# Kernel optimization log

Measured on AMD Instinct MI355X. Metric: run time of the kernel, lower is better.

Reference implementation:

```python
import jax, jax.numpy as jnp
import numpy as np
from functools import lru_cache
from jax.scipy.linalg import expm

N_QUBITS = 6
DIM = 2 ** N_QUBITS          # 64
N_PAULI = 4 ** N_QUBITS      # 4096


@lru_cache(maxsize=None)
def _pauli_tensor_np(n_qubits):
    # All n-qubit Pauli strings as dense matrices, ordered base-4
    # (digit 0..3 -> I, X, Y, Z; most-significant digit = first qubit).
    I = np.eye(2, dtype=np.complex64)
    X = np.array([[0, 1], [1, 0]], dtype=np.complex64)
    Y = np.array([[0, -1j], [1j, 0]], dtype=np.complex64)
    Z = np.array([[1, 0], [0, -1]], dtype=np.complex64)
    base = np.stack([I, X, Y, Z])  # [4,2,2]
    T = base
    for _ in range(n_qubits - 1):
        k, d = T.shape[0], T.shape[1]
        T = np.einsum('iab,jcd->ijacbd', T, base).reshape(k * 4, d * 2, d * 2)
    return np.ascontiguousarray(T.astype(np.complex64))  # [4^n, 2^n, 2^n]


def setup_inputs() -> dict:
    key = jax.random.key(0)
    kx, kw, kb = jax.random.split(key, 3)
    x = jax.random.normal(kx, (512, 4000), dtype=jnp.float32)
    weight = jax.random.normal(kw, (4, N_PAULI - 1), dtype=jnp.float32)
    bias = jax.random.normal(kb, (DIM,), dtype=jnp.float32)
    return {"x": x, "weight": weight, "bias": bias}


def reference(x, weight, bias):
    # x: [B, in_dim] float32; weight: [n_reps, 4^n - 1]; bias: [out_dim]
    B, in_dim = x.shape
    n_reps = weight.shape[0]
    out_dim = bias.shape[0]
    P = jnp.asarray(_pauli_tensor_np(N_QUBITS))  # [4096, 64, 64] complex64

    # Pad data coefficients up to the full Pauli basis (identity included).
    xp = jnp.pad(x, ((0, 0), (0, N_PAULI - in_dim))).astype(jnp.complex64)

    # Data-encoding Hamiltonian per sample: H_d[b] = sum_p x[b,p] * P[p]
    Hd = jnp.einsum('bp,pij->bij', xp, P)                       # [B,64,64]
    Ud = jax.vmap(expm)(-1j * Hd)                               # [B,64,64]

    # Trainable Hamiltonians per rep (identity Pauli excluded -> global phase).
    Hp = jnp.einsum('rp,pij->rij', weight.astype(jnp.complex64), P[1:])
    Up = jax.vmap(expm)(-1j * Hp)                               # [R,64,64]

    # Data re-uploading circuit on |0...0>: repeat (U_param @ U_data).
    psi = jnp.zeros((B, DIM), dtype=jnp.complex64).at[:, 0].set(1.0)
    for r in range(n_reps):
        psi = jnp.einsum('bij,bj->bi', Ud, psi)
        psi = jnp.einsum('ij,bj->bi', Up[r], psi)

    # Observables are computational-basis projectors |k><k|, k < out_dim:
    # <psi|O_k|psi> = |psi_k|^2
    probs = (psi[:, :out_dim].real ** 2 + psi[:, :out_dim].imag ** 2)
    return probs.astype(jnp.float32) + bias
```

## Files before the change

### kernel.cpp

```cpp
#include <hip/hip_runtime.h>
#include <math.h>

typedef float2 cplx;
typedef __attribute__((ext_vector_type(8))) short short8v;
typedef __attribute__((ext_vector_type(4))) short short4v;
typedef __attribute__((ext_vector_type(4))) float float4v;

#define IN_DIM 4000
#define NREPS 4

#define C0f  1.0f
#define C1f  1.0f
#define C2f  0.5f
#define C3f  0.16666667f
#define C4f  0.041666668f
#define C5f  8.3333333e-3f
#define C6f  1.3888889e-3f
#define C7f  1.9841270e-4f
#define C8f  2.4801587e-5f
#define C9f  2.7557319e-6f
#define C10f 2.7557319e-7f
#define C11f 2.5052108e-8f
#define C12f 2.0876757e-9f
#define C13f 1.6059044e-10f
#define C14f 1.1470746e-11f
#define C15f 7.6471637e-13f

#define MFMA(A,B,C) __builtin_amdgcn_mfma_f32_16x16x32_bf16((A),(B),(C),0,0,0)


__device__ __forceinline__ int idxSw(int a, int b) {
    return (a << 6) + ((((b >> 3) + a) & 7) << 3) + (b & 7);
}
__device__ __forceinline__ short f2bf(float f) {
    unsigned u = __float_as_uint(f);
    return (short)((u + 0x7FFF + ((u >> 16) & 1)) >> 16);
}
__device__ __forceinline__ float bf2f(short s) {
    return __uint_as_float(((unsigned)(unsigned short)s) << 16);
}
__device__ __forceinline__ short8v neg8(short8v a) {
    int4 u; __builtin_memcpy(&u, &a, 16);
    u.x ^= 0x80008000; u.y ^= 0x80008000; u.z ^= 0x80008000; u.w ^= 0x80008000;
    short8v r; __builtin_memcpy(&r, &u, 16); return r;
}

template<int AM, int BM, int ND>
__device__ __forceinline__ void mm_mfma(const short* __restrict__ As,
                                        const short* __restrict__ Bs,
                                        int li, int q, int mb, int nb,
                                        float4v* __restrict__ accR,
                                        float4v* __restrict__ accI)
{
    #pragma unroll
    for (int ks = 0; ks < 2; ks++) {
        const int ch = ks * 4 + q;
        short8v arh[ND], arl[ND], cRh[ND], cRl[ND], cIh[ND], cIl[ND];
        #pragma unroll
        for (int dm = 0; dm < ND; dm++) {
            int r = ((mb + dm) << 4) + li;
            int off = (r << 6) + (((ch + r) & 7) << 3);
            arh[dm] = *(const short8v*)(As + off);
            arl[dm] = *(const short8v*)(As + 4096 + off);
            short8v aih = *(const short8v*)(As + 8192 + off);
            short8v ail = *(const short8v*)(As + 12288 + off);
            short8v nih = neg8(aih), nil_ = neg8(ail);
            cRh[dm] = (AM == 2) ? aih : nih;
            cRl[dm] = (AM == 2) ? ail : nil_;
            cIh[dm] = (AM == 2) ? nih : aih;
            cIl[dm] = (AM == 2) ? nil_ : ail;
        }
        #pragma unroll
        for (int dn = 0; dn < ND; dn++) {
            int n = ((nb + dn) << 4) + li;
            int off = (n << 6) + (((ch + n) & 7) << 3);
            short8v brh = *(const short8v*)(Bs + off);
            short8v brl = *(const short8v*)(Bs + 4096 + off);
            short8v bih = *(const short8v*)(Bs + 8192 + off);
            short8v bil = *(const short8v*)(Bs + 12288 + off);
            if (BM == 1) { brh = neg8(brh); brl = neg8(brl); }
            #pragma unroll
            for (int dm = 0; dm < ND; dm++) {
                int ti = dm * ND + dn;
                accR[ti] = MFMA(arh[dm], brh, accR[ti]);
                accR[ti] = MFMA(arh[dm], brl, accR[ti]);
                accR[ti] = MFMA(arl[dm], brh, accR[ti]);
                accR[ti] = MFMA(cRh[dm], bih, accR[ti]);
                accR[ti] = MFMA(cRh[dm], bil, accR[ti]);
                accR[ti] = MFMA(cRl[dm], bih, accR[ti]);
                accI[ti] = MFMA(arh[dm], bih, accI[ti]);
                accI[ti] = MFMA(arh[dm], bil, accI[ti]);
                accI[ti] = MFMA(arl[dm], bih, accI[ti]);
                accI[ti] = MFMA(cIh[dm], brh, accI[ti]);
                accI[ti] = MFMA(cIh[dm], brl, accI[ti]);
                accI[ti] = MFMA(cIl[dm], brh, accI[ti]);
            }
        }
    }
}

template<int ND>
__device__ __forceinline__ void write_row(short* __restrict__ S, int li, int q,
                                          int mb, int nb,
                                          const float4v* cre, const float4v* cim)
{
    #pragma unroll
    for (int dm = 0; dm < ND; dm++)
    #pragma unroll
    for (int dn = 0; dn < ND; dn++) {
        int ti = dm * ND + dn;
        int c = ((nb + dn) << 4) + li;
        #pragma unroll
        for (int reg = 0; reg < 4; reg++) {
            int r = ((mb + dm) << 4) + q * 4 + reg;
            int off = idxSw(r, c);
            float vr = cre[ti][reg], vi = cim[ti][reg];
            short rh = f2bf(vr), rl = f2bf(vr - bf2f(rh));
            short ih = f2bf(vi), il = f2bf(vi - bf2f(ih));
            S[off] = rh; S[4096 + off] = rl; S[8192 + off] = ih; S[12288 + off] = il;
        }
    }
}

template<int ND>
__device__ __forceinline__ void write_rowT(short* __restrict__ S, int li, int q,
                                           int mb, int nb,
                                           const float4v* cre, const float4v* cim)
{
    #pragma unroll
    for (int dm = 0; dm < ND; dm++)
    #pragma unroll
    for (int dn = 0; dn < ND; dn++) {
        int ti = dm * ND + dn;
        int c = ((nb + dn) << 4) + li;
        int k0 = ((mb + dm) << 4) + q * 4;
        int off = idxSw(c, k0);
        short4v rh, rl, ih, il;
        #pragma unroll
        for (int reg = 0; reg < 4; reg++) {
            float vr = cre[ti][reg], vi = cim[ti][reg];
            short h1 = f2bf(vr); rh[reg] = h1; rl[reg] = f2bf(vr - bf2f(h1));
            short h2 = f2bf(vi); ih[reg] = h2; il[reg] = f2bf(vi - bf2f(h2));
        }
        *(short4v*)(S + off) = rh;
        *(short4v*)(S + 4096 + off) = rl;
        *(short4v*)(S + 8192 + off) = ih;
        *(short4v*)(S + 12288 + off) = il;
    }
}

template<int ND>
__device__ __forceinline__ void gather_tile(const short* __restrict__ S, int li, int q,
                                            int mb, int nb, float4v* bre, float4v* bim)
{
    #pragma unroll
    for (int dm = 0; dm < ND; dm++)
    #pragma unroll
    for (int dn = 0; dn < ND; dn++) {
        int ti = dm * ND + dn;
        int c = ((nb + dn) << 4) + li;
        #pragma unroll
        for (int reg = 0; reg < 4; reg++) {
            int r = ((mb + dm) << 4) + q * 4 + reg;
            int off = idxSw(r, c);
            bre[ti][reg] = bf2f(S[off]) + bf2f(S[4096 + off]);
            bim[ti][reg] = bf2f(S[8192 + off]) + bf2f(S[12288 + off]);
        }
    }
}

template<int ND>
__device__ __forceinline__ void adddiag(float4v* u, float cI, int li, int q, int mb, int nb)
{
    #pragma unroll
    for (int dm = 0; dm < ND; dm++)
    #pragma unroll
    for (int dn = 0; dn < ND; dn++) {
        if (mb + dm == nb + dn) {
            #pragma unroll
            for (int e = 0; e < 4; e++)
                if (li == q * 4 + e) u[dm * ND + dn][e] += cI;
        }
    }
}

template<int ND>
__device__ __forceinline__ void store_tiles(cplx* __restrict__ dst, int li, int q,
                                            int mb, int nb,
                                            const float4v* ure, const float4v* uim)
{
    #pragma unroll
    for (int dm = 0; dm < ND; dm++)
    #pragma unroll
    for (int dn = 0; dn < ND; dn++) {
        int ti = dm * ND + dn;
        int c = ((nb + dn) << 4) + li;
        int cs = c ^ (((c >> 4) & 1) << 1);
        #pragma unroll
        for (int reg = 0; reg < 4; reg++) {
            int r = ((mb + dm) << 4) + q * 4 + reg;
            dst[(r << 6) + cs] = make_float2(ure[ti][reg], uim[ti][reg]);
        }
    }
}

__device__ __forceinline__ cplx pauli_phase(float v, int xm, int zm) {
    int ny = __popc(xm & zm) & 3;
    if (ny == 0) return make_float2(v, 0.f);
    if (ny == 1) return make_float2(0.f, -v);
    if (ny == 2) return make_float2(-v, 0.f);
    return make_float2(0.f, v);
}

__device__ __forceinline__ void expm_core4(char* __restrict__ LDS,
                                           const float* __restrict__ src, bool isW,
                                           int t, float4v* ure, float4v* uim)
{
    constexpr int ND = 2, NT = 4;
    short* S0 = (short*)LDS;
    short* S1 = (short*)(LDS + 32768);
    cplx*  W  = (cplx*)(LDS + 32768);
    float* red = (float*)(LDS + 65536);
    const int lane = t & 63, wv = t >> 6;
    const int li = lane & 15, q = lane >> 4;
    const int mb = (wv & 1) << 1, nb = (wv >> 1) << 1;

    int xmt = 0, zmt = 0;
    #pragma unroll
    for (int k = 0; k < 6; k++) {
        int lo = (t >> (2 * k)) & 1, hi = (t >> (2 * k + 1)) & 1;
        zmt |= hi << k; xmt |= (hi ^ lo) << k;
    }
    float sumsq = 0.f;
    #pragma unroll
    for (int n = 0; n < 16; n++) {
        int p = t + 256 * n;
        int lo0 = n & 1, hi0 = (n >> 1) & 1, lo1 = (n >> 2) & 1, hi1 = (n >> 3) & 1;
        int zmn = hi0 | (hi1 << 1), xmn = (hi0 ^ lo0) | ((hi1 ^ lo1) << 1);
        int xm = xmt | (xmn << 4), zm = zmt | (zmn << 4);
        float v = isW ? ((p == 0) ? 0.f : src[p - 1])
                      : ((p < IN_DIM) ? src[p] : 0.f);
        sumsq += v * v;
        W[(xm << 6) + zm] = pauli_phase(v, xm, zm);
    }
    #pragma unroll
    for (int d = 32; d >= 1; d >>= 1) sumsq += __shfl_xor(sumsq, d, 64);
    if (lane == 0) red[wv] = sumsq;
    __syncthreads();

    float rs = 0.f;
    #pragma unroll
    for (int i2 = 0; i2 < 4; i2++) rs += red[i2];
    float fro = sqrtf(64.f * rs);
    int s1 = 0; { float nn = fro; while (nn > 8.f && s1 < 24) { nn *= 0.5f; s1++; } }
    float sc1 = exp2f((float)(-s1));

    cplx hv[16];
    #pragma unroll
    for (int rr = 0; rr < 16; rr++) hv[rr] = W[((wv * 16 + rr) << 6) + lane];
    #pragma unroll
    for (int d = 1; d < 64; d <<= 1) {
        float sg = (lane & d) ? -1.f : 1.f;
        #pragma unroll
        for (int rr = 0; rr < 16; rr++) {
            float px = __shfl_xor(hv[rr].x, d, 64);
            float py = __shfl_xor(hv[rr].y, d, 64);
            hv[rr].x = fmaf(sg, hv[rr].x, px);
            hv[rr].y = fmaf(sg, hv[rr].y, py);
        }
    }

    #pragma unroll
    for (int rr = 0; rr < 16; rr++) {
        int m = wv * 16 + rr;
        int c = lane ^ m;
        float vr = hv[rr].y * sc1, vi = -hv[rr].x * sc1;
        short rh = f2bf(vr), rl = f2bf(vr - bf2f(rh));
        short ih = f2bf(vi), il = f2bf(vi - bf2f(ih));
        int off = idxSw(lane, c);
        S0[off] = rh; S0[4096 + off] = rl; S0[8192 + off] = ih; S0[12288 + off] = il;
    }
    __syncthreads();

    const float4v z4 = {0.f, 0.f, 0.f, 0.f};
    float4v accR[NT], accI[NT];
    #define ZERO_ACC _Pragma("unroll") for (int i2 = 0; i2 < NT; i2++) { accR[i2]=z4; accI[i2]=z4; }

    ZERO_ACC
    mm_mfma<0, 1, ND>(S0, S0, li, q, mb, nb, accR, accI);
    float ss = 0.f;
    #pragma unroll
    for (int ti = 0; ti < NT; ti++)
        #pragma unroll
        for (int e = 0; e < 4; e++)
            ss += accR[ti][e]*accR[ti][e] + accI[ti][e]*accI[ti][e];
    #pragma unroll
    for (int d = 32; d >= 1; d >>= 1) ss += __shfl_xor(ss, d, 64);
    if (lane == 0) red[4 + wv] = ss;
    __syncthreads();

    rs = 0.f;
    #pragma unroll
    for (int i2 = 0; i2 < 4; i2++) rs += red[4 + i2];
    float bound = sqrtf(sqrtf(rs));
    int ds = 0; { float nn = bound; while (nn > 3.4f && ds < 12) { nn *= 0.5f; ds++; } }
    const int s = s1 + ds;
    float dsc = exp2f((float)(-ds)), dsc2 = dsc * dsc;

    float4v bre[NT], bim[NT];
    gather_tile<ND>(S0, li, q, mb, nb, bre, bim);
    float4v a2r[NT], a2i[NT];
    #pragma unroll
    for (int ti = 0; ti < NT; ti++) { a2r[ti] = accR[ti] * dsc2; a2i[ti] = accI[ti] * dsc2; }
    write_rowT<ND>(S1, li, q, mb, nb, a2r, a2i);
    __syncthreads();

    ZERO_ACC
    mm_mfma<2, 1, ND>(S1, S0, li, q, mb, nb, accR, accI);
    float4v a3r[NT], a3i[NT];
    #pragma unroll
    for (int ti = 0; ti < NT; ti++) { a3r[ti] = accR[ti] * dsc; a3i[ti] = accI[ti] * dsc; }
    ZERO_ACC
    mm_mfma<2, 0, ND>(S1, S1, li, q, mb, nb, accR, accI);
    __syncthreads();
    write_rowT<ND>(S0, li, q, mb, nb, accR, accI);
    {
        float caA = C13f * dsc, ca3 = C15f * dsc;
        #pragma unroll
        for (int ti = 0; ti < NT; ti++) {
            ure[ti] = caA * bre[ti] + C14f * a2r[ti] + ca3 * a3r[ti];
            uim[ti] = caA * bim[ti] + C14f * a2i[ti] + ca3 * a3i[ti];
        }
        adddiag<ND>(ure, C12f, li, q, mb, nb);
        write_row<ND>(S1, li, q, mb, nb, ure, uim);
    }
    __syncthreads();

    const float cIc[3] = { C0f, C4f, C8f };
    const float cAc[3] = { C1f, C5f, C9f };
    const float c2c[3] = { C2f, C6f, C10f };
    const float c3c[3] = { C3f, C7f, C11f };
    for (int j = 2; j >= 0; j--) {
        ZERO_ACC
        mm_mfma<0, 0, ND>(S1, S0, li, q, mb, nb, accR, accI);
        __syncthreads();
        float caA = cAc[j] * dsc, ca3 = c3c[j] * dsc;
        #pragma unroll
        for (int ti = 0; ti < NT; ti++) {
            ure[ti] = accR[ti] + caA * bre[ti] + c2c[j] * a2r[ti] + ca3 * a3r[ti];
            uim[ti] = accI[ti] + caA * bim[ti] + c2c[j] * a2i[ti] + ca3 * a3i[ti];
        }
        adddiag<ND>(ure, cIc[j], li, q, mb, nb);
        write_row<ND>(S1, li, q, mb, nb, ure, uim);
        if (j == 0) write_rowT<ND>(S0, li, q, mb, nb, ure, uim);
        __syncthreads();
    }

    for (int sq = 0; sq < s; sq++) {
        if (sq > 0) {
            write_row<ND>(S1, li, q, mb, nb, ure, uim);
            write_rowT<ND>(S0, li, q, mb, nb, ure, uim);
            __syncthreads();
        }
        ZERO_ACC
        mm_mfma<0, 0, ND>(S1, S0, li, q, mb, nb, accR, accI);
        __syncthreads();
        #pragma unroll
        for (int ti = 0; ti < NT; ti++) { ure[ti] = accR[ti]; uim[ti] = accI[ti]; }
    }
    #undef ZERO_ACC
}

__device__ __forceinline__ cplx matvec_wave(const cplx* __restrict__ M,
                                            const cplx* __restrict__ pin,
                                            int lane, int wv)
{
    const int rr = (wv << 4) + (lane & 15);
    const int kc = lane >> 4;
    float ax = 0.f, ay = 0.f;
    const float4* Mr = (const float4*)(M + (rr << 6));
    #pragma unroll
    for (int c = 0; c < 4; c++) {
        int ch = ((kc << 2) + c + rr) & 15;
        int b = (ch >> 2) & 1;
        float4 m01 = Mr[(ch << 1) + b];
        float4 m23 = Mr[(ch << 1) + 1 - b];
        const cplx* p = pin + (ch << 2);
        cplx p0 = p[0], p1 = p[1], p2 = p[2], p3 = p[3];
        ax = fmaf(m01.x, p0.x, fmaf(-m01.y, p0.y, ax));
        ay = fmaf(m01.x, p0.y, fmaf( m01.y, p0.x, ay));
        ax = fmaf(m01.z, p1.x, fmaf(-m01.w, p1.y, ax));
        ay = fmaf(m01.z, p1.y, fmaf( m01.w, p1.x, ay));
        ax = fmaf(m23.x, p2.x, fmaf(-m23.y, p2.y, ax));
        ay = fmaf(m23.x, p2.y, fmaf( m23.y, p2.x, ay));
        ax = fmaf(m23.z, p3.x, fmaf(-m23.w, p3.y, ax));
        ay = fmaf(m23.z, p3.y, fmaf( m23.w, p3.x, ay));
    }
    ax += __shfl_xor(ax, 16, 64); ay += __shfl_xor(ay, 16, 64);
    ax += __shfl_xor(ax, 32, 64); ay += __shfl_xor(ay, 32, 64);
    return make_float2(ax, ay);
}

__global__ __launch_bounds__(256, 2) void circuit_kernel(const float* __restrict__ x,
                                                         const float* __restrict__ w,
                                                         const float* __restrict__ bias,
                                                         cplx* __restrict__ ws,
                                                         int* __restrict__ flag,
                                                         float* __restrict__ out)
{
    __shared__ float4 LDSf4[4168];
    char* LDS = (char*)LDSf4;
    const int t = threadIdx.x, b = blockIdx.x;
    const int lane = t & 63, wv = t >> 6, li = lane & 15, q = lane >> 4;
    float4v ure[4], uim[4];

    if (b < NREPS) {
        expm_core4(LDS, w + (size_t)b * 4095, true, t, ure, uim);
        store_tiles<2>(ws + ((size_t)b << 12), li, q, (wv & 1) << 1, (wv >> 1) << 1,
                       ure, uim);
        __syncthreads();
        if (t == 0)
            __hip_atomic_fetch_add(flag, 1, __ATOMIC_RELEASE, __HIP_MEMORY_SCOPE_AGENT);
    }

    expm_core4(LDS, x + (size_t)b * IN_DIM, false, t, ure, uim);

    cplx* Ud   = (cplx*)(LDS + 32768);
    cplx* UpS  = (cplx*)LDS;
    cplx* psiA = (cplx*)(LDS + 65664);
    cplx* psiB = (cplx*)(LDS + 66176);

    store_tiles<2>(Ud, li, q, (wv & 1) << 1, (wv >> 1) << 1, ure, uim);
    if (t < 64) psiA[t] = make_float2(t == 0 ? 1.f : 0.f, 0.f);
    if (t == 0) {
        while (__hip_atomic_load(flag, __ATOMIC_ACQUIRE, __HIP_MEMORY_SCOPE_AGENT) < NREPS)
            __builtin_amdgcn_s_sleep(8);
    }
    __syncthreads();

    const int rowi = (wv << 4) + (lane & 15);
    for (int r = 0; r < NREPS; r++) {
        {
            const float4* srcv = (const float4*)(ws + ((size_t)r << 12));
            float4* dstY = (float4*)UpS;
            #pragma unroll
            for (int n = 0; n < 8; n++) dstY[n * 256 + t] = srcv[n * 256 + t];
        }
        cplx v1 = matvec_wave(Ud, psiA, lane, wv);
        if (lane < 16) psiB[rowi] = v1;
        __syncthreads();
        cplx v2 = matvec_wave(UpS, psiB, lane, wv);
        if (lane < 16) psiA[rowi] = v2;
        __syncthreads();
    }
    if (t < 64) {
        cplx pv = psiA[t];
        out[(b << 6) + t] = fmaf(pv.x, pv.x, fmaf(pv.y, pv.y, bias[t]));
    }
}

extern "C" void kernel_launch(void* const* d_in, const int* in_sizes, int n_in,
                              void* d_out, int out_size, void* d_ws, size_t ws_size,
                              hipStream_t stream)
{
    const float* x    = (const float*)d_in[0];
    const float* w    = (const float*)d_in[1];
    const float* bias = (const float*)d_in[2];
    float* out = (float*)d_out;
    cplx* ws   = (cplx*)d_ws;
    int* flag  = (int*)((char*)d_ws + (NREPS << 15));

    int B = in_sizes[0] / IN_DIM;

    hipMemsetAsync(flag, 0, sizeof(int), stream);
    hipLaunchKernelGGL(circuit_kernel, dim3(B), dim3(256), 0, stream,
                       x, w, bias, ws, flag, out);
}
```

Measured before the change: 166.6 us.

## Use Horner Taylor evaluation in expm, add MFMA priority, loop expm duties

Measured after the change: 197.7 us. +18.7%, slower.

```diff
diff --git a/kernel.cpp b/kernel.cpp
--- a/kernel.cpp
+++ b/kernel.cpp
@@ -79,6 +79,7 @@
             short8v bih = *(const short8v*)(Bs + 8192 + off);
             short8v bil = *(const short8v*)(Bs + 12288 + off);
             if (BM == 1) { brh = neg8(brh); brl = neg8(brl); }
+            __builtin_amdgcn_s_setprio(1);
             #pragma unroll
             for (int dm = 0; dm < ND; dm++) {
                 int ti = dm * ND + dn;
@@ -95,6 +96,7 @@
                 accI[ti] = MFMA(cIh[dm], brl, accI[ti]);
                 accI[ti] = MFMA(cIl[dm], brh, accI[ti]);
             }
+            __builtin_amdgcn_s_setprio(0);
         }
     }
 }
@@ -309,59 +311,42 @@
 
     float4v bre[NT], bim[NT];
     gather_tile<ND>(S0, li, q, mb, nb, bre, bim);
-    float4v a2r[NT], a2i[NT];
-    #pragma unroll
-    for (int ti = 0; ti < NT; ti++) { a2r[ti] = accR[ti] * dsc2; a2i[ti] = accI[ti] * dsc2; }
-    write_rowT<ND>(S1, li, q, mb, nb, a2r, a2i);
-    __syncthreads();
-
-    ZERO_ACC
-    mm_mfma<2, 1, ND>(S1, S0, li, q, mb, nb, accR, accI);
-    float4v a3r[NT], a3i[NT];
-    #pragma unroll
-    for (int ti = 0; ti < NT; ti++) { a3r[ti] = accR[ti] * dsc; a3i[ti] = accI[ti] * dsc; }
-    ZERO_ACC
-    mm_mfma<2, 0, ND>(S1, S1, li, q, mb, nb, accR, accI);
-    __syncthreads();
-    write_rowT<ND>(S0, li, q, mb, nb, accR, accI);
+
+    #pragma unroll
+    for (int ti = 0; ti < NT; ti++) { ure[ti] = accR[ti] * dsc2; uim[ti] = accI[ti] * dsc2; }
+    write_rowT<ND>(S1, li, q, mb, nb, ure, uim);
+    __syncthreads();
+
     {
-        float caA = C13f * dsc, ca3 = C15f * dsc;
+        float ca = C15f * dsc;
+        #pragma unroll
+        for (int ti = 0; ti < NT; ti++) { ure[ti] = ca * bre[ti]; uim[ti] = ca * bim[ti]; }
+        adddiag<ND>(ure, C14f, li, q, mb, nb);
+        write_rowT<ND>(S0, li, q, mb, nb, ure, uim);
+    }
+    __syncthreads();
+
+    const float cIc[7] = { C0f, C2f, C4f, C6f, C8f, C10f, C12f };
+    const float cAc[7] = { C1f, C3f, C5f, C7f, C9f, C11f, C13f };
+    for (int j = 6; j >= 0; j--) {
+        ZERO_ACC
+        mm_mfma<2, 0, ND>(S1, S0, li, q, mb, nb, accR, accI);
+        __syncthreads();
+        float ca = cAc[j] * dsc, cI = cIc[j];
         #pragma unroll
         for (int ti = 0; ti < NT; ti++) {
-            ure[ti] = caA * bre[ti] + C14f * a2r[ti] + ca3 * a3r[ti];
-            uim[ti] = caA * bim[ti] + C14f * a2i[ti] + ca3 * a3i[ti];
-        }
-        adddiag<ND>(ure, C12f, li, q, mb, nb);
+            ure[ti] = accR[ti] + ca * bre[ti];
+            uim[ti] = accI[ti] + ca * bim[ti];
+        }
+        adddiag<ND>(ure, cI, li, q, mb, nb);
+        write_rowT<ND>(S0, li, q, mb, nb, ure, uim);
+        __syncthreads();
+    }
+
+    for (int sq = 0; sq < s; sq++) {
         write_row<ND>(S1, li, q, mb, nb, ure, uim);
-    }
-    __syncthreads();
-
-    const float cIc[3] = { C0f, C4f, C8f };
-    const float cAc[3] = { C1f, C5f, C9f };
-    const float c2c[3] = { C2f, C6f, C10f };
-    const float c3c[3] = { C3f, C7f, C11f };
-    for (int j = 2; j >= 0; j--) {
-        ZERO_ACC
-        mm_mfma<0, 0, ND>(S1, S0, li, q, mb, nb, accR, accI);
-        __syncthreads();
-        float caA = cAc[j] * dsc, ca3 = c3c[j] * dsc;
-        #pragma unroll
-        for (int ti = 0; ti < NT; ti++) {
-            ure[ti] = accR[ti] + caA * bre[ti] + c2c[j] * a2r[ti] + ca3 * a3r[ti];
-            uim[ti] = accI[ti] + caA * bim[ti] + c2c[j] * a2i[ti] + ca3 * a3i[ti];
-        }
-        adddiag<ND>(ure, cIc[j], li, q, mb, nb);
-        write_row<ND>(S1, li, q, mb, nb, ure, uim);
-        if (j == 0) write_rowT<ND>(S0, li, q, mb, nb, ure, uim);
-        __syncthreads();
-    }
-
-    for (int sq = 0; sq < s; sq++) {
-        if (sq > 0) {
-            write_row<ND>(S1, li, q, mb, nb, ure, uim);
-            write_rowT<ND>(S0, li, q, mb, nb, ure, uim);
-            __syncthreads();
-        }
+        if (sq > 0) write_rowT<ND>(S0, li, q, mb, nb, ure, uim);
+        __syncthreads();
         ZERO_ACC
         mm_mfma<0, 0, ND>(S1, S0, li, q, mb, nb, accR, accI);
         __syncthreads();
@@ -401,12 +386,12 @@
     return make_float2(ax, ay);
 }
 
-__global__ __launch_bounds__(256, 2) void circuit_kernel(const float* __restrict__ x,
-                                                         const float* __restrict__ w,
-                                                         const float* __restrict__ bias,
-                                                         cplx* __restrict__ ws,
-                                                         int* __restrict__ flag,
-                                                         float* __restrict__ out)
+__global__ __launch_bounds__(256) void circuit_kernel(const float* __restrict__ x,
+                                                      const float* __restrict__ w,
+                                                      const float* __restrict__ bias,
+                                                      cplx* __restrict__ ws,
+                                                      int* __restrict__ flag,
+                                                      float* __restrict__ out)
 {
     __shared__ float4 LDSf4[4168];
     char* LDS = (char*)LDSf4;
@@ -414,16 +399,18 @@
     const int lane = t & 63, wv = t >> 6, li = lane & 15, q = lane >> 4;
     float4v ure[4], uim[4];
 
-    if (b < NREPS) {
-        expm_core4(LDS, w + (size_t)b * 4095, true, t, ure, uim);
-        store_tiles<2>(ws + ((size_t)b << 12), li, q, (wv & 1) << 1, (wv >> 1) << 1,
-                       ure, uim);
-        __syncthreads();
-        if (t == 0)
-            __hip_atomic_fetch_add(flag, 1, __ATOMIC_RELEASE, __HIP_MEMORY_SCOPE_AGENT);
-    }
-
-    expm_core4(LDS, x + (size_t)b * IN_DIM, false, t, ure, uim);
+    for (int duty = (b < NREPS) ? 0 : 1; duty < 2; duty++) {
+        const bool isW = (duty == 0);
+        const float* src = isW ? (w + (size_t)b * 4095) : (x + (size_t)b * IN_DIM);
+        expm_core4(LDS, src, isW, t, ure, uim);
+        if (isW) {
+            store_tiles<2>(ws + ((size_t)b << 12), li, q, (wv & 1) << 1,
+                           (wv >> 1) << 1, ure, uim);
+            __syncthreads();
+            if (t == 0)
+                __hip_atomic_fetch_add(flag, 1, __ATOMIC_RELEASE, __HIP_MEMORY_SCOPE_AGENT);
+        }
+    }
 
     cplx* Ud   = (cplx*)(LDS + 32768);
     cplx* UpS  = (cplx*)LDS;
```
